# Optimization experiments

Hardware: AMD Instinct MI355X
Metric: run time of the kernel (lower is better)

## Reference

```python
import jax, jax.numpy as jnp
import numpy as np
import math

B, H, S, D = 1, 8, 2048, 64
LAMBDA_INIT = 0.8 - 0.6 * math.exp(-0.3)  # depth=1
EPS = 1e-5


def _clin(xr, xi, wr, wi, br, bi):
    # complex linear: (wr + i*wi)(xr + i*xi)
    out_r = xr @ wr.T - xi @ wi.T + br
    out_i = xr @ wi.T + xi @ wr.T + bi
    return out_r, out_i


def setup_inputs() -> dict:
    ks = jax.random.split(jax.random.key(0), 24)
    n = lambda i, shp, s=1.0: jax.random.normal(ks[i], shp, jnp.float32) * s
    inv = 1.0 / math.sqrt(D)
    return {
        'q_r': n(0, (B, H, S, D)), 'q_i': n(1, (B, H, S, D)),
        'k_r': n(2, (B, H, S, D)), 'k_i': n(3, (B, H, S, D)),
        'v_r': n(4, (B, H, S, D)), 'v_i': n(5, (B, H, S, D)),
        'pe_q_r': n(6, (B, H, S, D)), 'pe_q_i': n(7, (B, H, S, D)),
        'pe_k_r': n(8, (B, H, S, D)), 'pe_k_i': n(9, (B, H, S, D)),
        'qwr': n(10, (2 * D, D), inv), 'qwi': n(11, (2 * D, D), inv),
        'qbr': jnp.zeros(2 * D), 'qbi': jnp.zeros(2 * D),
        'kwr': n(12, (D, D), inv), 'kwi': n(13, (D, D), inv),
        'kbr': jnp.zeros(D), 'kbi': jnp.zeros(D),
        'vwr': n(14, (D, D), inv), 'vwi': n(15, (D, D), inv),
        'vbr': jnp.zeros(D), 'vbi': jnp.zeros(D),
        'gwr': n(16, (D, D), inv), 'gwi': n(17, (D, D), inv),
        'gbr': jnp.zeros(D), 'gbi': jnp.zeros(D),
        'owr': n(18, (D, D), inv), 'owi': n(19, (D, D), inv),
        'obr': jnp.zeros(D), 'obi': jnp.zeros(D),
        'lq1': n(20, (H,), 0.1), 'lk1': n(21, (H,), 0.1),
        'lq2': n(22, (H,), 0.1), 'lk2': n(23, (H,), 0.1),
        'subw': jnp.ones(2 * D),
    }


def _forward(q_r, q_i, k_r, k_i, v_r, v_i, pe_q_r, pe_q_i, pe_k_r, pe_k_i,
             qwr, qwi, qbr, qbi, kwr, kwi, kbr, kbi, vwr, vwi, vbr, vbi,
             gwr, gwi, gbr, gbi, owr, owi, obr, obi,
             lq1, lk1, lq2, lk2, subw):
    b, h, s, d = q_r.shape
    scale = d ** (-0.5)
    qpr, qpi = _clin(q_r, q_i, qwr, qwi, qbr, qbi)      # [b,h,s,2d]
    kpr, kpi = _clin(k_r, k_i, kwr, kwi, kbr, kbi)      # [b,h,s,d]
    vpr, vpi = _clin(v_r, v_i, vwr, vwi, vbr, vbi)      # [b,h,s,d]
    qpr = qpr + jnp.concatenate([pe_q_r, pe_q_r], -1)
    qpi = qpi + jnp.concatenate([pe_q_i, pe_q_i], -1)
    kpr = kpr + pe_k_r
    kpi = kpi + pe_k_i
    # split two physical heads: view(..., d, 2) interleaves last dim
    qpr = qpr.reshape(b, h, s, d, 2)
    qpi = qpi.reshape(b, h, s, d, 2)
    q1r, q2r = qpr[..., 0], qpr[..., 1]
    q1i, q2i = qpi[..., 0], qpi[..., 1]

    def attn(qr, qi):
        sr = jnp.einsum('bhqd,bhkd->bhqk', qr, kpr) + jnp.einsum('bhqd,bhkd->bhqk', qi, kpi)
        si = jnp.einsum('bhqd,bhkd->bhqk', qi, kpr) - jnp.einsum('bhqd,bhkd->bhqk', qr, kpi)
        scores = jnp.sqrt(sr * sr + si * si + 1e-8) * scale
        return jax.nn.softmax(scores, axis=-1)

    a1 = attn(q1r, q1i)
    a2 = attn(q2r, q2i)
    o1r = a1 @ vpr; o1i = a1 @ vpi
    o2r = a2 @ vpr; o2i = a2 @ vpi
    # NOTE: torch computes a lambda-weighted difference here but immediately
    # overwrites it with the normed slice below, so it never reaches the output.
    cr = jnp.stack([o1r, o2r], -1).reshape(b, h, s, 2 * d)
    ci = jnp.stack([o1i, o2i], -1).reshape(b, h, s, 2 * d)
    rms = jnp.sqrt(jnp.mean(cr * cr + ci * ci, axis=-1, keepdims=True) + EPS)
    nr = cr / rms * subw
    ni = ci / rms * subw
    ar = nr[..., :d]
    ai = ni[..., :d]
    gr, gi = _clin(q_r, q_i, gwr, gwi, gbr, gbi)
    xr = gr * ar - gi * ai
    xi = gr * ai + gi * ar
    out_r, out_i = _clin(xr, xi, owr, owi, obr, obi)
    return out_r, out_i, gr, gi


def reference(q_r, q_i, k_r, k_i, v_r, v_i, pe_q_r, pe_q_i, pe_k_r, pe_k_i,
              qwr, qwi, qbr, qbi, kwr, kwi, kbr, kbi, vwr, vwi, vbr, vbi,
              gwr, gwi, gbr, gbi, owr, owi, obr, obi,
              lq1, lk1, lq2, lk2, subw):
    return _forward(q_r, q_i, k_r, k_i, v_r, v_i, pe_q_r, pe_q_i, pe_k_r, pe_k_i,
                    qwr, qwi, qbr, qbi, kwr, kwi, kbr, kbi, vwr, vwi, vbr, vbi,
                    gwr, gwi, gbr, gbi, owr, owi, obr, obi,
                    lq1, lk1, lq2, lk2, subw)
```

## Files before the change

kernel.cpp:

```cpp
#include <hip/hip_runtime.h>
#include <hip/hip_bf16.h>

#define NH 8
#define SQ 2048
#define HD 64
#define NTOT (NH * SQ * HD)

typedef unsigned short u16;
typedef unsigned int u32;
typedef __attribute__((ext_vector_type(8))) unsigned short us8;
typedef __attribute__((ext_vector_type(4))) unsigned short us4v;
typedef __attribute__((ext_vector_type(8))) _Float16 h8;
typedef __attribute__((ext_vector_type(4))) float f4;
typedef __attribute__((ext_vector_type(4))) u32 u4;

#define MFMA_F16 __builtin_amdgcn_mfma_f32_16x16x32_f16

__device__ __forceinline__ u16 f2h(float f) {
    union { _Float16 h; u16 u; } c; c.h = (_Float16)f; return c.u;
}
__device__ __forceinline__ float h2f(u16 u) {
    union { _Float16 h; u16 u; } c; c.u = u; return (float)c.h;
}
__device__ __forceinline__ h8 neg_h8(h8 a) {
    union { h8 h; u4 u; } c; c.h = a;
    c.u ^= 0x80008000u;
    return c.h;
}
__device__ __forceinline__ h8 pack8h(const float* p) {
    float4 a = ((const float4*)p)[0];
    float4 b = ((const float4*)p)[1];
    h8 r;
    r[0] = (_Float16)a.x; r[1] = (_Float16)a.y; r[2] = (_Float16)a.z; r[3] = (_Float16)a.w;
    r[4] = (_Float16)b.x; r[5] = (_Float16)b.y; r[6] = (_Float16)b.z; r[7] = (_Float16)b.w;
    return r;
}

__device__ __forceinline__ int swz8(int row, int chunk) {
    return row * 64 + ((chunk ^ (row & 7)) << 3);
}

struct Afrag { h8 r0, r1, i0, i1, ni0, ni1; };

__global__ __launch_bounds__(128) void prep_kernel(
    const float* __restrict__ qwr, const float* __restrict__ qwi,
    const float* __restrict__ kwr, const float* __restrict__ kwi,
    const float* __restrict__ vwr, const float* __restrict__ vwi,
    const float* __restrict__ gwr, const float* __restrict__ gwi,
    const float* __restrict__ owr, const float* __restrict__ owi,
    u16* __restrict__ pk)
{
    const int b = blockIdx.x;
    const float* W; int nt;
    if (b < 8)       { W = qwr; nt = b; }
    else if (b < 16) { W = qwi; nt = b - 8; }
    else if (b < 20) { W = kwr; nt = b - 16; }
    else if (b < 24) { W = kwi; nt = b - 20; }
    else if (b < 28) { W = vwr; nt = b - 24; }
    else if (b < 32) { W = vwi; nt = b - 28; }
    else if (b < 36) { W = gwr; nt = b - 32; }
    else if (b < 40) { W = gwi; nt = b - 36; }
    else if (b < 44) { W = owr; nt = b - 40; }
    else             { W = owi; nt = b - 44; }
    const int t = threadIdx.x, hf = t >> 6, l = t & 63;
    const int quad = l >> 4, m16 = l & 15;
    h8 v = pack8h(W + (nt * 16 + m16) * 64 + hf * 32 + quad * 8);
    *(h8*)(pk + b * 1024 + hf * 512 + l * 8) = v;
}

__global__ __launch_bounds__(256) void proj_kernel(
    const float* __restrict__ q_r, const float* __restrict__ q_i,
    const float* __restrict__ k_r, const float* __restrict__ k_i,
    const float* __restrict__ v_r, const float* __restrict__ v_i,
    const float* __restrict__ pe_q_r, const float* __restrict__ pe_q_i,
    const float* __restrict__ pe_k_r, const float* __restrict__ pe_k_i,
    const u16* __restrict__ pk,
    const float* __restrict__ qbr, const float* __restrict__ qbi,
    const float* __restrict__ kbr, const float* __restrict__ kbi,
    const float* __restrict__ vbr, const float* __restrict__ vbi,
    const float* __restrict__ gbr, const float* __restrict__ gbi,
    u16* __restrict__ q1r, u16* __restrict__ q1i,
    u16* __restrict__ q2r, u16* __restrict__ q2i,
    u16* __restrict__ kpr, u16* __restrict__ kpi,
    u16* __restrict__ vtr, u16* __restrict__ vti,
    float* __restrict__ out_gr, float* __restrict__ out_gi)
{
    __shared__ __align__(16) u16 Sqr[16 * 64], Sqi[16 * 64];
    __shared__ __align__(16) u16 Skr[16 * 64], Ski[16 * 64];
    __shared__ __align__(16) u16 Svr[16 * 64], Svi[16 * 64];
    __shared__ __align__(16) u16 Oq1r[16 * 68], Oq1i[16 * 68];
    __shared__ __align__(16) u16 Oq2r[16 * 68], Oq2i[16 * 68];
    __shared__ __align__(16) u16 Okr[16 * 68],  Oki[16 * 68];
    __shared__ __align__(16) float Ogr[16 * 68], Ogi[16 * 68];

    const int t = threadIdx.x;
    const int wv = t >> 6, l = t & 63;
    const int quad = l >> 4, m16 = l & 15;
    const int rowbase = blockIdx.x * 16;
    const int h = rowbase >> 11;
    const int l8 = l * 8;

    {
        const int r = t >> 4, c4 = (t & 15) * 4;
        const int off = swz8(r, c4 >> 3) + (c4 & 7);
        const size_t gi = (size_t)(rowbase + r) * 64 + c4;
        auto stage = [&](const float* src, u16* dst) {
            float4 v = *(const float4*)(src + gi);
            us4v p;
            p[0] = f2h(v.x); p[1] = f2h(v.y); p[2] = f2h(v.z); p[3] = f2h(v.w);
            *(us4v*)&dst[off] = p;
        };
        stage(q_r, Sqr); stage(q_i, Sqi);
        stage(k_r, Skr); stage(k_i, Ski);
        stage(v_r, Svr); stage(v_i, Svi);
    }
    __syncthreads();

    auto loadA = [&](const u16* Sr, const u16* Si) {
        Afrag a;
        a.r0 = *(const h8*)&Sr[swz8(m16, quad)];
        a.r1 = *(const h8*)&Sr[swz8(m16, quad + 4)];
        a.i0 = *(const h8*)&Si[swz8(m16, quad)];
        a.i1 = *(const h8*)&Si[swz8(m16, quad + 4)];
        a.ni0 = neg_h8(a.i0);
        a.ni1 = neg_h8(a.i1);
        return a;
    };

    auto ctile = [&](const Afrag& A, int planeR, int planeI, f4& Cr, f4& Ci) {
        const u16* pR = pk + planeR * 1024;
        const u16* pI = pk + planeI * 1024;
        h8 Br0 = *(const h8*)(pR + l8);
        h8 Br1 = *(const h8*)(pR + 512 + l8);
        h8 Bi0 = *(const h8*)(pI + l8);
        h8 Bi1 = *(const h8*)(pI + 512 + l8);
        Cr = (f4)0.f; Ci = (f4)0.f;
        Cr = MFMA_F16(A.r0,  Br0, Cr, 0, 0, 0);
        Cr = MFMA_F16(A.r1,  Br1, Cr, 0, 0, 0);
        Cr = MFMA_F16(A.ni0, Bi0, Cr, 0, 0, 0);
        Cr = MFMA_F16(A.ni1, Bi1, Cr, 0, 0, 0);
        Ci = MFMA_F16(A.r0,  Bi0, Ci, 0, 0, 0);
        Ci = MFMA_F16(A.r1,  Bi1, Ci, 0, 0, 0);
        Ci = MFMA_F16(A.i0,  Br0, Ci, 0, 0, 0);
        Ci = MFMA_F16(A.i1,  Br1, Ci, 0, 0, 0);
    };

    auto qtile = [&](const Afrag& A, int nt) {
        f4 Cr, Ci;
        ctile(A, nt, 8 + nt, Cr, Ci);
        int c = nt * 16 + m16;
        float br = qbr[c], bi = qbi[c];
        int dd = c >> 1, pc = c & 63;
        u16* dR = (c & 1) ? Oq2r : Oq1r;
        u16* dI = (c & 1) ? Oq2i : Oq1i;
        #pragma unroll
        for (int r = 0; r < 4; ++r) {
            int row = quad * 4 + r;
            int g = rowbase + row;
            dR[row * 68 + dd] = f2h(Cr[r] + br + pe_q_r[g * 64 + pc]);
            dI[row * 68 + dd] = f2h(Ci[r] + bi + pe_q_i[g * 64 + pc]);
        }
    };
    auto ktile = [&](const Afrag& A, int nt) {
        f4 Cr, Ci;
        ctile(A, 16 + nt, 20 + nt, Cr, Ci);
        int c = nt * 16 + m16;
        float br = kbr[c], bi = kbi[c];
        #pragma unroll
        for (int r = 0; r < 4; ++r) {
            int row = quad * 4 + r;
            int g = rowbase + row;
            Okr[row * 68 + c] = f2h(Cr[r] + br + pe_k_r[g * 64 + c]);
            Oki[row * 68 + c] = f2h(Ci[r] + bi + pe_k_i[g * 64 + c]);
        }
    };
    auto vtile = [&](const Afrag& A, int nt) {
        f4 Cr, Ci;
        ctile(A, 24 + nt, 28 + nt, Cr, Ci);
        int c = nt * 16 + m16;
        float br = vbr[c], bi = vbi[c];
        int s0 = (rowbase & 2047) + quad * 4;
        size_t tix = (size_t)(h * 64 + c) * 2048 + s0;
        us4v pr, pi;
        #pragma unroll
        for (int r = 0; r < 4; ++r) {
            pr[r] = f2h(Cr[r] + br);
            pi[r] = f2h(Ci[r] + bi);
        }
        *(us4v*)&vtr[tix] = pr;
        *(us4v*)&vti[tix] = pi;
    };
    auto gtile = [&](const Afrag& A, int nt) {
        f4 Cr, Ci;
        ctile(A, 32 + nt, 36 + nt, Cr, Ci);
        int c = nt * 16 + m16;
        float br = gbr[c], bi = gbi[c];
        #pragma unroll
        for (int r = 0; r < 4; ++r) {
            int row = quad * 4 + r;
            Ogr[row * 68 + c] = Cr[r] + br;
            Ogi[row * 68 + c] = Ci[r] + bi;
        }
    };

    if (wv == 0) {
        Afrag Aq = loadA(Sqr, Sqi);
        qtile(Aq, 0); qtile(Aq, 1); qtile(Aq, 2); qtile(Aq, 3); qtile(Aq, 4);
    } else if (wv == 1) {
        Afrag Aq = loadA(Sqr, Sqi);
        qtile(Aq, 5); qtile(Aq, 6); qtile(Aq, 7);
        gtile(Aq, 0); gtile(Aq, 1);
    } else if (wv == 2) {
        Afrag Ak = loadA(Skr, Ski);
        ktile(Ak, 0); ktile(Ak, 1); ktile(Ak, 2); ktile(Ak, 3);
        Afrag Aq = loadA(Sqr, Sqi);
        gtile(Aq, 2);
    } else {
        Afrag Av = loadA(Svr, Svi);
        vtile(Av, 0); vtile(Av, 1); vtile(Av, 2); vtile(Av, 3);
        Afrag Aq = loadA(Sqr, Sqi);
        gtile(Aq, 3);
    }
    __syncthreads();

    {
        const int r = t >> 4, c4 = (t & 15) * 4;
        const size_t gi = (size_t)(rowbase + r) * 64 + c4;
        const int lo = r * 68 + c4;
        *(us4v*)&q1r[gi] = *(const us4v*)&Oq1r[lo];
        *(us4v*)&q1i[gi] = *(const us4v*)&Oq1i[lo];
        *(us4v*)&q2r[gi] = *(const us4v*)&Oq2r[lo];
        *(us4v*)&q2i[gi] = *(const us4v*)&Oq2i[lo];
        *(us4v*)&kpr[gi] = *(const us4v*)&Okr[lo];
        *(us4v*)&kpi[gi] = *(const us4v*)&Oki[lo];
        *(float4*)&out_gr[gi] = *(const float4*)&Ogr[lo];
        *(float4*)&out_gi[gi] = *(const float4*)&Ogi[lo];
    }
}

__global__ __launch_bounds__(512, 1) void attn_kernel(
    const u16* __restrict__ q1r, const u16* __restrict__ q1i,
    const u16* __restrict__ q2r, const u16* __restrict__ q2i,
    const u16* __restrict__ kpr, const u16* __restrict__ kpi,
    const u16* __restrict__ vtr, const u16* __restrict__ vti,
    const u16* __restrict__ pk,
    const float* __restrict__ subw,
    const float* __restrict__ obr, const float* __restrict__ obi,
    const float* __restrict__ out_gr, const float* __restrict__ out_gi,
    float* __restrict__ out_r, float* __restrict__ out_i)
{
    __shared__ __align__(16) u16 Kr[2][64 * 64], Ki[2][64 * 64];
    __shared__ __align__(16) u16 Vr[2][64 * 64], Vi[2][64 * 64];
    __shared__ __align__(16) u16 Pb[128 * 64];
    __shared__ float ssL[2][64];

    const int t  = threadIdx.x;
    const int qt = blockIdx.x;
    const int h  = blockIdx.z;

    const int wq   = t >> 6;
    const int br   = wq >> 2;
    const int wr   = wq & 3;
    const int l    = t & 63;
    const int quad = l >> 4;
    const int m    = l & 15;

    const u16* Qsr = br ? q2r : q1r;
    const u16* Qsi = br ? q2i : q1i;
    const int hbase = h * SQ * 64;
    const int qbase = hbase + qt * 64 * 64;
    const int vbase = h * 64 * SQ;

    const u16* qrr = Qsr + qbase + (wr * 16 + m) * 64;
    const u16* qri = Qsi + qbase + (wr * 16 + m) * 64;
    h8 Qr0 = *(const h8*)(qrr + quad * 8);
    h8 Qr1 = *(const h8*)(qrr + 32 + quad * 8);
    h8 Qi0 = *(const h8*)(qri + quad * 8);
    h8 Qi1 = *(const h8*)(qri + 32 + quad * 8);

    const int sr0 = t >> 3;
    const int sc  = t & 7;
    us8 rK, rC, rV, rW;

    auto issue = [&](int kt) {
        const int kb = hbase + kt * 4096;
        const int vb = vbase + kt * 64;
        const int sc8 = sc * 8;
        rK = *(const us8*)(kpr + kb + sr0 * 64 + sc8);
        rC = *(const us8*)(kpi + kb + sr0 * 64 + sc8);
        rV = *(const us8*)(vtr + vb + sr0 * SQ + sc8);
        rW = *(const us8*)(vti + vb + sr0 * SQ + sc8);
    };
    auto commit = [&](int b) {
        const int o = swz8(sr0, sc);
        *(us8*)&Kr[b][o] = rK;
        *(us8*)&Ki[b][o] = rC;
        *(us8*)&Vr[b][o] = rV;
        *(us8*)&Vi[b][o] = rW;
    };

    float mreg = -1e30f, Lp = 0.f;
    f4 Ovr[4], Ovi[4];
    #pragma unroll
    for (int d = 0; d < 4; ++d) { Ovr[d] = (f4)0.f; Ovi[d] = (f4)0.f; }

    issue(0);
    commit(0);
    issue(1);
    __syncthreads();

    const int prow = wq * 16 + m;

    for (int kt = 0; kt < 32; ++kt) {
        const int cur = kt & 1;
        if (kt < 31) commit(cur ^ 1);
        if (kt < 30) issue(kt + 2);

        float sv[4][4];
        #pragma unroll
        for (int nt = 0; nt < 4; ++nt) {
            const int kr = nt * 16 + m;
            h8 k0 = *(const h8*)&Kr[cur][swz8(kr, quad)];
            h8 k1 = *(const h8*)&Kr[cur][swz8(kr, quad + 4)];
            h8 c0 = *(const h8*)&Ki[cur][swz8(kr, quad)];
            h8 c1 = *(const h8*)&Ki[cur][swz8(kr, quad + 4)];
            h8 nc0 = neg_h8(c0);
            h8 nc1 = neg_h8(c1);
            f4 ar = (f4)0.f, ai = (f4)0.f;
            __builtin_amdgcn_s_setprio(1);
            ar = MFMA_F16(k0,  Qr0, ar, 0, 0, 0);
            ar = MFMA_F16(k1,  Qr1, ar, 0, 0, 0);
            ar = MFMA_F16(c0,  Qi0, ar, 0, 0, 0);
            ar = MFMA_F16(c1,  Qi1, ar, 0, 0, 0);
            ai = MFMA_F16(k0,  Qi0, ai, 0, 0, 0);
            ai = MFMA_F16(k1,  Qi1, ai, 0, 0, 0);
            ai = MFMA_F16(nc0, Qr0, ai, 0, 0, 0);
            ai = MFMA_F16(nc1, Qr1, ai, 0, 0, 0);
            __builtin_amdgcn_s_setprio(0);
            #pragma unroll
            for (int r = 0; r < 4; ++r)
                sv[nt][r] = __builtin_amdgcn_sqrtf(ar[r] * ar[r] + ai[r] * ai[r] + 1e-8f) * 0.125f;
        }

        float a0 = fmaxf(fmaxf(sv[0][0], sv[0][1]), fmaxf(sv[0][2], sv[0][3]));
        float a1 = fmaxf(fmaxf(sv[1][0], sv[1][1]), fmaxf(sv[1][2], sv[1][3]));
        float a2 = fmaxf(fmaxf(sv[2][0], sv[2][1]), fmaxf(sv[2][2], sv[2][3]));
        float a3 = fmaxf(fmaxf(sv[3][0], sv[3][1]), fmaxf(sv[3][2], sv[3][3]));
        float rv = fmaxf(fmaxf(a0, a1), fmaxf(a2, a3));
        rv = fmaxf(rv, __shfl_xor(rv, 16));
        rv = fmaxf(rv, __shfl_xor(rv, 32));

        if (__any(rv > mreg + 8.f)) {
            float mn = fmaxf(mreg, rv);
            float al = __expf(mreg - mn);
            mreg = mn;
            Lp *= al;
            #pragma unroll
            for (int r = 0; r < 4; ++r) {
                float alr = __shfl(al, quad * 4 + r);
                #pragma unroll
                for (int dt = 0; dt < 4; ++dt) { Ovr[dt][r] *= alr; Ovi[dt][r] *= alr; }
            }
        }

        #pragma unroll
        for (int nt = 0; nt < 4; ++nt) {
            us4v pw;
            #pragma unroll
            for (int r = 0; r < 4; ++r) {
                float p = __expf(sv[nt][r] - mreg);
                Lp += p;
                pw[r] = f2h(p);
            }
            *(us4v*)&Pb[swz8(prow, 2 * nt + (quad >> 1)) + ((quad & 1) << 2)] = pw;
        }

        h8 pa0 = *(const h8*)&Pb[swz8(prow, quad)];
        h8 pa1 = *(const h8*)&Pb[swz8(prow, quad + 4)];

        #pragma unroll
        for (int dt = 0; dt < 4; ++dt) {
            const int vr_ = dt * 16 + m;
            h8 b0 = *(const h8*)&Vr[cur][swz8(vr_, quad)];
            h8 b1 = *(const h8*)&Vr[cur][swz8(vr_, quad + 4)];
            h8 d0 = *(const h8*)&Vi[cur][swz8(vr_, quad)];
            h8 d1 = *(const h8*)&Vi[cur][swz8(vr_, quad + 4)];
            __builtin_amdgcn_s_setprio(1);
            Ovr[dt] = MFMA_F16(pa0, b0, Ovr[dt], 0, 0, 0);
            Ovr[dt] = MFMA_F16(pa1, b1, Ovr[dt], 0, 0, 0);
            Ovi[dt] = MFMA_F16(pa0, d0, Ovi[dt], 0, 0, 0);
            Ovi[dt] = MFMA_F16(pa1, d1, Ovi[dt], 0, 0, 0);
            __builtin_amdgcn_s_setprio(0);
        }

        __syncthreads();
    }

    {
        float x = Lp;
        x += __shfl_xor(x, 16);
        x += __shfl_xor(x, 32);
        float invq = 1.f / x;
        #pragma unroll
        for (int r = 0; r < 4; ++r) {
            float inv = __shfl(invq, quad * 4 + r);
            #pragma unroll
            for (int dt = 0; dt < 4; ++dt) { Ovr[dt][r] *= inv; Ovi[dt][r] *= inv; }
        }

        float ssp[4];
        #pragma unroll
        for (int r = 0; r < 4; ++r) {
            float s = 0.f;
            #pragma unroll
            for (int dt = 0; dt < 4; ++dt)
                s += Ovr[dt][r] * Ovr[dt][r] + Ovi[dt][r] * Ovi[dt][r];
            s += __shfl_xor(s, 1);
            s += __shfl_xor(s, 2);
            s += __shfl_xor(s, 4);
            s += __shfl_xor(s, 8);
            ssp[r] = s;
        }
        if (m == 0) {
            #pragma unroll
            for (int r = 0; r < 4; ++r)
                ssL[br][wr * 16 + quad * 4 + r] = ssp[r];
        }
        __syncthreads();

        float rmi[4];
        #pragma unroll
        for (int r = 0; r < 4; ++r) {
            const int row = wr * 16 + quad * 4 + r;
            float ss = ssL[0][row] + ssL[1][row];
            rmi[r] = 1.f / sqrtf(ss * (1.f / 128.f) + 1e-5f);
        }

        u16* Xr = Pb;
        u16* Xi = Pb + 4096;
        const int growb = h * 2048 + qt * 64;
        #pragma unroll
        for (int dt = 0; dt < 2; ++dt) {
            const int k = dt * 16 + m;
            const int c = 2 * k + br;
            const float sw = subw[c];
            #pragma unroll
            for (int r = 0; r < 4; ++r) {
                const int row = wr * 16 + quad * 4 + r;
                const size_t gidx = (size_t)(growb + row) * 64 + c;
                float g_r = out_gr[gidx];
                float g_i = out_gi[gidx];
                float a_r = Ovr[dt][r] * rmi[r] * sw;
                float a_i = Ovi[dt][r] * rmi[r] * sw;
                const int off = swz8(row, c >> 3) + (c & 7);
                Xr[off] = f2h(g_r * a_r - g_i * a_i);
                Xi[off] = f2h(g_r * a_i + g_i * a_r);
            }
        }
        __syncthreads();

        const int ct  = wq & 3;
        const int rh2 = wq >> 2;
        const int c   = ct * 16 + m;
        const float br_ = obr[c], bi_ = obi[c];
        const u16* pR = pk + (40 + ct) * 1024;
        const u16* pI = pk + (44 + ct) * 1024;
        h8 Br0 = *(const h8*)(pR + l * 8);
        h8 Br1 = *(const h8*)(pR + 512 + l * 8);
        h8 Bi0 = *(const h8*)(pI + l * 8);
        h8 Bi1 = *(const h8*)(pI + 512 + l * 8);

        #pragma unroll
        for (int rt = 0; rt < 2; ++rt) {
            const int arow = rh2 * 32 + rt * 16 + m;
            h8 Ar0 = *(const h8*)&Xr[swz8(arow, quad)];
            h8 Ar1 = *(const h8*)&Xr[swz8(arow, quad + 4)];
            h8 Ai0 = *(const h8*)&Xi[swz8(arow, quad)];
            h8 Ai1 = *(const h8*)&Xi[swz8(arow, quad + 4)];
            h8 nAi0 = neg_h8(Ai0), nAi1 = neg_h8(Ai1);

            f4 Cr = (f4)0.f, Ci = (f4)0.f;
            Cr = MFMA_F16(Ar0,  Br0, Cr, 0, 0, 0);
            Cr = MFMA_F16(Ar1,  Br1, Cr, 0, 0, 0);
            Cr = MFMA_F16(nAi0, Bi0, Cr, 0, 0, 0);
            Cr = MFMA_F16(nAi1, Bi1, Cr, 0, 0, 0);
            Ci = MFMA_F16(Ar0,  Bi0, Ci, 0, 0, 0);
            Ci = MFMA_F16(Ar1,  Bi1, Ci, 0, 0, 0);
            Ci = MFMA_F16(Ai0,  Br0, Ci, 0, 0, 0);
            Ci = MFMA_F16(Ai1,  Br1, Ci, 0, 0, 0);

            #pragma unroll
            for (int r = 0; r < 4; ++r) {
                const int row = rh2 * 32 + rt * 16 + quad * 4 + r;
                const size_t g = (size_t)(growb + row) * 64 + c;
                out_r[g] = Cr[r] + br_;
                out_i[g] = Ci[r] + bi_;
            }
        }
    }
}

extern "C" void kernel_launch(void* const* d_in, const int* in_sizes, int n_in,
                              void* d_out, int out_size, void* d_ws, size_t ws_size,
                              hipStream_t stream)
{
    (void)in_sizes; (void)n_in; (void)out_size; (void)ws_size;

    float* out    = (float*)d_out;
    float* out_r  = out;
    float* out_i  = out + (size_t)NTOT;
    float* out_gr = out + 2 * (size_t)NTOT;
    float* out_gi = out + 3 * (size_t)NTOT;

    char* w = (char*)d_ws;
    const size_t N = (size_t)NTOT;
    u16* q1r = (u16*)w; w += N * 2;
    u16* q1i = (u16*)w; w += N * 2;
    u16* q2r = (u16*)w; w += N * 2;
    u16* q2i = (u16*)w; w += N * 2;
    u16* kpr = (u16*)w; w += N * 2;
    u16* kpi = (u16*)w; w += N * 2;
    u16* vtr = (u16*)w; w += N * 2;
    u16* vti = (u16*)w; w += N * 2;
    u16* pk  = (u16*)w;

    prep_kernel<<<dim3(48), dim3(128), 0, stream>>>(
        (const float*)d_in[10], (const float*)d_in[11],
        (const float*)d_in[14], (const float*)d_in[15],
        (const float*)d_in[18], (const float*)d_in[19],
        (const float*)d_in[22], (const float*)d_in[23],
        (const float*)d_in[26], (const float*)d_in[27],
        pk);

    proj_kernel<<<dim3(1024), dim3(256), 0, stream>>>(
        (const float*)d_in[0], (const float*)d_in[1],
        (const float*)d_in[2], (const float*)d_in[3],
        (const float*)d_in[4], (const float*)d_in[5],
        (const float*)d_in[6], (const float*)d_in[7],
        (const float*)d_in[8], (const float*)d_in[9],
        pk,
        (const float*)d_in[12], (const float*)d_in[13],
        (const float*)d_in[16], (const float*)d_in[17],
        (const float*)d_in[20], (const float*)d_in[21],
        (const float*)d_in[24], (const float*)d_in[25],
        q1r, q1i, q2r, q2i, kpr, kpi, vtr, vti, out_gr, out_gi);

    attn_kernel<<<dim3(SQ / 64, 1, NH), dim3(512), 0, stream>>>(
        q1r, q1i, q2r, q2i, kpr, kpi, vtr, vti,
        pk, (const float*)d_in[34],
        (const float*)d_in[28], (const float*)d_in[29],
        out_gr, out_gi, out_r, out_i);
}
```

Baseline: 224.5 us.

## Triple-buffer K/V LDS tiles and prefetch next K fragments into registers

Replaces the double-buffered K/V shared-memory tiles with a three-stage ring. The commit of tile kt+2 moves to after the PV MFMAs, and the K fragments for the next tile are loaded from LDS into registers during the softmax phase. This is meant to hide the global-load latency and the LDS read latency behind compute. In exchange it raises LDS use by another 32 KB stage and adds 16 h8 fragment registers per thread, which may cause register pressure or spills at 512 threads per block.

```diff
diff --git a/kernel.cpp b/kernel.cpp
--- a/kernel.cpp
+++ b/kernel.cpp
@@ -249,8 +249,7 @@
     const float* __restrict__ out_gr, const float* __restrict__ out_gi,
     float* __restrict__ out_r, float* __restrict__ out_i)
 {
-    __shared__ __align__(16) u16 Kr[2][64 * 64], Ki[2][64 * 64];
-    __shared__ __align__(16) u16 Vr[2][64 * 64], Vi[2][64 * 64];
+    __shared__ __align__(16) u16 TILE[3][4][4096];
     __shared__ __align__(16) u16 Pb[128 * 64];
     __shared__ float ssL[2][64];
 
@@ -291,12 +290,26 @@
         rV = *(const us8*)(vtr + vb + sr0 * SQ + sc8);
         rW = *(const us8*)(vti + vb + sr0 * SQ + sc8);
     };
-    auto commit = [&](int b) {
+    auto commit = [&](int s) {
         const int o = swz8(sr0, sc);
-        *(us8*)&Kr[b][o] = rK;
-        *(us8*)&Ki[b][o] = rC;
-        *(us8*)&Vr[b][o] = rV;
-        *(us8*)&Vi[b][o] = rW;
+        *(us8*)&TILE[s][0][o] = rK;
+        *(us8*)&TILE[s][1][o] = rC;
+        *(us8*)&TILE[s][2][o] = rV;
+        *(us8*)&TILE[s][3][o] = rW;
+    };
+
+    h8 kf0[4], kf1[4], cf0[4], cf1[4];
+    auto prefetchK = [&](int s) {
+        const u16* KrS = TILE[s][0];
+        const u16* KiS = TILE[s][1];
+        #pragma unroll
+        for (int nt = 0; nt < 4; ++nt) {
+            const int kr = nt * 16 + m;
+            kf0[nt] = *(const h8*)&KrS[swz8(kr, quad)];
+            kf1[nt] = *(const h8*)&KrS[swz8(kr, quad + 4)];
+            cf0[nt] = *(const h8*)&KiS[swz8(kr, quad)];
+            cf1[nt] = *(const h8*)&KiS[swz8(kr, quad + 4)];
+        }
     };
 
     float mreg = -1e30f, Lp = 0.f;
@@ -307,40 +320,38 @@
     issue(0);
     commit(0);
     issue(1);
+    commit(1);
     __syncthreads();
+    prefetchK(0);
 
     const int prow = wq * 16 + m;
 
     for (int kt = 0; kt < 32; ++kt) {
-        const int cur = kt & 1;
-        if (kt < 31) commit(cur ^ 1);
+        const int cur = kt % 3;
         if (kt < 30) issue(kt + 2);
 
         float sv[4][4];
         #pragma unroll
         for (int nt = 0; nt < 4; ++nt) {
-            const int kr = nt * 16 + m;
-            h8 k0 = *(const h8*)&Kr[cur][swz8(kr, quad)];
-            h8 k1 = *(const h8*)&Kr[cur][swz8(kr, quad + 4)];
-            h8 c0 = *(const h8*)&Ki[cur][swz8(kr, quad)];
-            h8 c1 = *(const h8*)&Ki[cur][swz8(kr, quad + 4)];
-            h8 nc0 = neg_h8(c0);
-            h8 nc1 = neg_h8(c1);
+            h8 nc0 = neg_h8(cf0[nt]);
+            h8 nc1 = neg_h8(cf1[nt]);
             f4 ar = (f4)0.f, ai = (f4)0.f;
             __builtin_amdgcn_s_setprio(1);
-            ar = MFMA_F16(k0,  Qr0, ar, 0, 0, 0);
-            ar = MFMA_F16(k1,  Qr1, ar, 0, 0, 0);
-            ar = MFMA_F16(c0,  Qi0, ar, 0, 0, 0);
-            ar = MFMA_F16(c1,  Qi1, ar, 0, 0, 0);
-            ai = MFMA_F16(k0,  Qi0, ai, 0, 0, 0);
-            ai = MFMA_F16(k1,  Qi1, ai, 0, 0, 0);
-            ai = MFMA_F16(nc0, Qr0, ai, 0, 0, 0);
-            ai = MFMA_F16(nc1, Qr1, ai, 0, 0, 0);
+            ar = MFMA_F16(kf0[nt], Qr0, ar, 0, 0, 0);
+            ar = MFMA_F16(kf1[nt], Qr1, ar, 0, 0, 0);
+            ar = MFMA_F16(cf0[nt], Qi0, ar, 0, 0, 0);
+            ar = MFMA_F16(cf1[nt], Qi1, ar, 0, 0, 0);
+            ai = MFMA_F16(kf0[nt], Qi0, ai, 0, 0, 0);
+            ai = MFMA_F16(kf1[nt], Qi1, ai, 0, 0, 0);
+            ai = MFMA_F16(nc0,     Qr0, ai, 0, 0, 0);
+            ai = MFMA_F16(nc1,     Qr1, ai, 0, 0, 0);
             __builtin_amdgcn_s_setprio(0);
             #pragma unroll
             for (int r = 0; r < 4; ++r)
                 sv[nt][r] = __builtin_amdgcn_sqrtf(ar[r] * ar[r] + ai[r] * ai[r] + 1e-8f) * 0.125f;
         }
+
+        if (kt < 31) prefetchK((kt + 1) % 3);
 
         float a0 = fmaxf(fmaxf(sv[0][0], sv[0][1]), fmaxf(sv[0][2], sv[0][3]));
         float a1 = fmaxf(fmaxf(sv[1][0], sv[1][1]), fmaxf(sv[1][2], sv[1][3]));
@@ -378,13 +389,15 @@
         h8 pa0 = *(const h8*)&Pb[swz8(prow, quad)];
         h8 pa1 = *(const h8*)&Pb[swz8(prow, quad + 4)];
 
+        const u16* VrS = TILE[cur][2];
+        const u16* ViS = TILE[cur][3];
         #pragma unroll
         for (int dt = 0; dt < 4; ++dt) {
             const int vr_ = dt * 16 + m;
-            h8 b0 = *(const h8*)&Vr[cur][swz8(vr_, quad)];
-            h8 b1 = *(const h8*)&Vr[cur][swz8(vr_, quad + 4)];
-            h8 d0 = *(const h8*)&Vi[cur][swz8(vr_, quad)];
-            h8 d1 = *(const h8*)&Vi[cur][swz8(vr_, quad + 4)];
+            h8 b0 = *(const h8*)&VrS[swz8(vr_, quad)];
+            h8 b1 = *(const h8*)&VrS[swz8(vr_, quad + 4)];
+            h8 d0 = *(const h8*)&ViS[swz8(vr_, quad)];
+            h8 d1 = *(const h8*)&ViS[swz8(vr_, quad + 4)];
             __builtin_amdgcn_s_setprio(1);
             Ovr[dt] = MFMA_F16(pa0, b0, Ovr[dt], 0, 0, 0);
             Ovr[dt] = MFMA_F16(pa1, b1, Ovr[dt], 0, 0, 0);
@@ -392,6 +405,8 @@
             Ovi[dt] = MFMA_F16(pa1, d1, Ovi[dt], 0, 0, 0);
             __builtin_amdgcn_s_setprio(0);
         }
+
+        if (kt < 30) commit((kt + 2) % 3);
 
         __syncthreads();
     }
```

Result: slower. 234.7 us (+4.6%).
